# Kernel tuning notes

Measured on AMD Instinct MI355X. Metric: run time of the kernel, lower is better.

Reference implementation:

```python
import jax, jax.numpy as jnp
import numpy as np

N, E, F_IN, F_E = 50000, 800000, 128, 16
R, H, C = 4, 4, 32            # num_relations, heads, out_channels
HC = H * C                     # 128
NEG_SLOPE = 0.2                # PyG RGATConv default negative_slope
EPS = 1e-16                    # PyG softmax epsilon


def rgat_conv(x, src, dst, edge_type, edge_attr, w, q, k, e, le, b, concat):
    """Faithful PyG RGATConv (additive-self-attention, across-relation, dim=1, aggr=add).
    x: [N,F]; w: [R,F,H*C]; q,k,e: [H*C,H]; le: [F_e,H*C]; b: bias."""
    n = x.shape[0]
    xw = jnp.einsum('nf,rfo->rno', x, w)              # [R,N,H*C] per-relation projections
    x_i = xw[edge_type, dst]                          # [E,H*C] target-node proj per edge
    x_j = xw[edge_type, src]                          # [E,H*C] source-node proj per edge
    qi = x_i @ q                                      # [E,H]
    kj = x_j @ k + (edge_attr @ le) @ e               # [E,H] (edge features folded into keys)
    alpha = jax.nn.leaky_relu(qi + kj, NEG_SLOPE)     # [E,H]
    # softmax over incoming edges of each destination node (across relations)
    amax = jax.ops.segment_max(alpha, dst, num_segments=n)
    ex = jnp.exp(alpha - amax[dst])
    denom = jax.ops.segment_sum(ex, dst, num_segments=n)
    alpha = ex / (denom[dst] + EPS)
    msg = alpha[:, :, None] * x_j.reshape(-1, H, C)   # [E,H,C]
    out = jax.ops.segment_sum(msg, dst, num_segments=n)  # [N,H,C] sum aggregation
    out = out.reshape(n, H * C) if concat else out.mean(axis=1)
    return out + b


def setup_inputs() -> dict:
    key = jax.random.key(0)
    ks = jax.random.split(key, 18)
    p = 0.05
    inp = {
        'x': jax.random.normal(ks[0], (N, F_IN), dtype=jnp.float32),
        'edge_index': jax.random.randint(ks[1], (2, E), 0, N, dtype=jnp.int64)
            if jax.config.jax_enable_x64 else jax.random.randint(ks[1], (2, E), 0, N).astype(jnp.int32),
        'edge_attr': jax.random.normal(ks[2], (E, F_E), dtype=jnp.float32),
        'edge_type': jax.random.randint(ks[3], (E,), 0, R).astype(jnp.int32),
        # conv1 params (in=F_IN, concat=True -> bias of size H*C)
        'w1': jax.random.normal(ks[4], (R, F_IN, HC), dtype=jnp.float32) * p,
        'q1': jax.random.normal(ks[5], (HC, H), dtype=jnp.float32) * p,
        'k1': jax.random.normal(ks[6], (HC, H), dtype=jnp.float32) * p,
        'e1': jax.random.normal(ks[7], (HC, H), dtype=jnp.float32) * p,
        'le1': jax.random.normal(ks[8], (F_E, HC), dtype=jnp.float32) * p,
        'b1': jnp.zeros((HC,), dtype=jnp.float32),
        # conv3 params (in=H*C=128, concat=False -> bias of size C)
        'w3': jax.random.normal(ks[9], (R, HC, HC), dtype=jnp.float32) * p,
        'q3': jax.random.normal(ks[10], (HC, H), dtype=jnp.float32) * p,
        'k3': jax.random.normal(ks[11], (HC, H), dtype=jnp.float32) * p,
        'e3': jax.random.normal(ks[12], (HC, H), dtype=jnp.float32) * p,
        'le3': jax.random.normal(ks[13], (F_E, HC), dtype=jnp.float32) * p,
        'b3': jnp.zeros((C,), dtype=jnp.float32),
    }
    return inp


def reference(x, edge_index, edge_attr, edge_type,
              w1, q1, k1, e1, le1, b1,
              w3, q3, k3, e3, le3, b3):
    src, dst = edge_index[0], edge_index[1]
    h = jax.nn.relu(rgat_conv(x, src, dst, edge_type, edge_attr,
                              w1, q1, k1, e1, le1, b1, concat=True))
    out = rgat_conv(h, src, dst, edge_type, edge_attr,
                    w3, q3, k3, e3, le3, b3, concat=False)
    return out
```

## Files before the change

### kernel.cpp

```cpp
#include <hip/hip_runtime.h>


#define NEG_SLOPE 0.2f
#define SOFT_EPS 1e-16f
#define SRC_MASK 0x07FFFFFF

typedef __attribute__((ext_vector_type(8))) short bf16x8;
typedef __attribute__((ext_vector_type(4))) float f32x4;
typedef __attribute__((ext_vector_type(4))) unsigned short u16x4;
typedef __attribute__((ext_vector_type(4))) _Float16 half4;
typedef __attribute__((ext_vector_type(8))) _Float16 half8;

__device__ __forceinline__ void bf16split(float f, unsigned short& h, unsigned short& l) {
  unsigned u = __float_as_uint(f);
  unsigned r = u + 0x7FFFu + ((u >> 16) & 1u);
  h = (unsigned short)(r >> 16);
  float fh = __uint_as_float(((unsigned)h) << 16);
  float d = f - fh;
  unsigned u2 = __float_as_uint(d);
  unsigned r2 = u2 + 0x7FFFu + ((u2 >> 16) & 1u);
  l = (unsigned short)(r2 >> 16);
}


__device__ __forceinline__ void hist_body(int id, const int* __restrict__ dst,
                                          int* __restrict__ deg, int E) {
  int e = id * 256 + (int)threadIdx.x;
  if (e < E) atomicAdd(&deg[dst[e]], 1);
}

__device__ __forceinline__ void convx_body(int id, const float* __restrict__ in,
                                           unsigned short* __restrict__ hi,
                                           unsigned short* __restrict__ lo, int total8) {
  int i = id * 256 + (int)threadIdx.x;
  if (i >= total8) return;
  const float4* p = (const float4*)in + (size_t)i * 2;
  float4 a = p[0], b = p[1];
  float v[8] = {a.x, a.y, a.z, a.w, b.x, b.y, b.z, b.w};
  bf16x8 hv, lv;
#pragma unroll
  for (int j = 0; j < 8; ++j) {
    unsigned short h, l;
    bf16split(v[j], h, l);
    hv[j] = (short)h; lv[j] = (short)l;
  }
  *(bf16x8*)(hi + (size_t)i * 8) = hv;
  *(bf16x8*)(lo + (size_t)i * 8) = lv;
}

__device__ __forceinline__ void ekp_body(int id, const float* __restrict__ ea,
                                         const float* __restrict__ le1, const float* __restrict__ e1,
                                         const float* __restrict__ le3, const float* __restrict__ e3,
                                         float* __restrict__ eks1, float* __restrict__ eks3,
                                         int E) {
  __shared__ float sl[128];
  int t = threadIdx.x;
  if (t < 128) {
    const float* le = (t < 64) ? le1 : le3;
    const float* ee = (t < 64) ? e1 : e3;
    int u = t & 63, f = u >> 2, h = u & 3;
    float acc = 0.f;
    for (int o = 0; o < 128; ++o) acc += le[f * 128 + o] * ee[o * 4 + h];
    sl[t] = acc;
  }
  __syncthreads();
  int i = id * 256 + t;
  if (i >= E) return;
  const float4* a4 = (const float4*)(ea + (size_t)i * 16);
  float a1[4] = {0, 0, 0, 0}, a3[4] = {0, 0, 0, 0};
#pragma unroll
  for (int ii = 0; ii < 4; ++ii) {
    float4 v = a4[ii];
    int f = ii * 4;
#pragma unroll
    for (int h = 0; h < 4; ++h) {
      a1[h] += v.x * sl[f * 4 + h] + v.y * sl[(f + 1) * 4 + h] +
               v.z * sl[(f + 2) * 4 + h] + v.w * sl[(f + 3) * 4 + h];
      a3[h] += v.x * sl[64 + f * 4 + h] + v.y * sl[64 + (f + 1) * 4 + h] +
               v.z * sl[64 + (f + 2) * 4 + h] + v.w * sl[64 + (f + 3) * 4 + h];
    }
  }
  *(float4*)(eks1 + (size_t)i * 4) = make_float4(a1[0], a1[1], a1[2], a1[3]);
  *(float4*)(eks3 + (size_t)i * 4) = make_float4(a3[0], a3[1], a3[2], a3[3]);
}

__device__ __forceinline__ void convw_body(int idx, const float* __restrict__ w1,
                                           const float* __restrict__ w3,
                                           unsigned short* __restrict__ wF1h,
                                           unsigned short* __restrict__ wF1l,
                                           unsigned short* __restrict__ wF3h,
                                           unsigned short* __restrict__ wF3l) {
  if (idx >= 131072) return;
  int L = idx >> 16;
  int rem = idx & 65535;
  int r = rem >> 14, rem2 = rem & 16383, f = rem2 >> 7, o = rem2 & 127;
  const float* w = L ? w3 : w1;
  unsigned short* dh = L ? wF3h : wF1h;
  unsigned short* dl = L ? wF3l : wF1l;
  float v = w[(r * 128 + f) * 128 + o];
  unsigned short h, l;
  bf16split(v, h, l);
  int ot = o >> 4, c = o & 15, kc = f >> 5, q = (f >> 3) & 3, j = f & 7;
  int di = r * 16384 + ((((ot * 4 + kc) * 4 + q) * 16 + c) * 8 + j);
  dh[di] = h;
  dl[di] = l;
}

__device__ __forceinline__ void wqk_body(int idx, const float* __restrict__ w1,
                                         const float* __restrict__ q1, const float* __restrict__ k1,
                                         const float* __restrict__ w3, const float* __restrict__ q3,
                                         const float* __restrict__ k3, float* __restrict__ wqk) {
  if (idx >= 8192) return;
  int L = idx >> 12, rem = idx & 4095;
  int r = rem >> 10, rem2 = rem & 1023, f = rem2 >> 3, j = rem2 & 7;
  const float* w = L ? w3 : w1;
  const float* qk = (j < 4) ? (L ? q3 : q1) : (L ? k3 : k1);
  int h = j & 3;
  const float* wrow = w + (r * 128 + f) * 128;
  float acc = 0.f;
  for (int o = 0; o < 128; ++o) acc += wrow[o] * qk[o * 4 + h];
  wqk[idx] = acc;
}

__global__ __launch_bounds__(256) void pre_kernel(
    const int* __restrict__ dst, int* __restrict__ deg, int E,
    const float* __restrict__ x, unsigned short* __restrict__ xhi,
    unsigned short* __restrict__ xlo, int total8,
    const float* __restrict__ ea,
    const float* __restrict__ le1, const float* __restrict__ e1,
    const float* __restrict__ le3, const float* __restrict__ e3,
    float* __restrict__ eks1, float* __restrict__ eks3,
    const float* __restrict__ w1, const float* __restrict__ q1, const float* __restrict__ k1,
    const float* __restrict__ w3, const float* __restrict__ q3, const float* __restrict__ k3,
    float* __restrict__ wqk,
    unsigned short* __restrict__ wF1h, unsigned short* __restrict__ wF1l,
    unsigned short* __restrict__ wF3h, unsigned short* __restrict__ wF3l,
    int nABC, int eb, int cxb) {
  int bid = blockIdx.x;
  if (bid < nABC) {
    int id = bid / 3, r3 = bid - id * 3;
    if (r3 == 0) {
      if (id < eb) hist_body(id, dst, deg, E);
    } else if (r3 == 1) {
      if (id < cxb) convx_body(id, x, xhi, xlo, total8);
    } else {
      if (id < eb) ekp_body(id, ea, le1, e1, le3, e3, eks1, eks3, E);
    }
  } else {
    int b2 = bid - nABC;
    if (b2 < 512) {
      convw_body(b2 * 256 + (int)threadIdx.x, w1, w3, wF1h, wF1l, wF3h, wF3l);
    } else {
      wqk_body((b2 - 512) * 256 + (int)threadIdx.x, w1, q1, k1, w3, q3, k3, wqk);
    }
  }
}


__global__ __launch_bounds__(256) void scanA_kernel(const int* __restrict__ deg,
                                                    int* __restrict__ bsum, int N) {
  int b = blockIdx.x, t = threadIdx.x;
  int base = b * 1024 + t * 4;
  int s = 0;
#pragma unroll
  for (int j = 0; j < 4; ++j) {
    int i = base + j;
    if (i < N) s += deg[i];
  }
#pragma unroll
  for (int o = 1; o < 64; o <<= 1) s += __shfl_xor(s, o);
  __shared__ int wsum[4];
  if ((t & 63) == 0) wsum[t >> 6] = s;
  __syncthreads();
  if (t == 0) bsum[b] = wsum[0] + wsum[1] + wsum[2] + wsum[3];
}

__global__ __launch_bounds__(256) void scanB_kernel(const int* __restrict__ bsum,
                                                    int* __restrict__ boff,
                                                    int* __restrict__ row_start,
                                                    int nb, int N) {
  int t = threadIdx.x;
  int v = (t < nb) ? bsum[t] : 0;
  int inc = v;
#pragma unroll
  for (int o = 1; o < 64; o <<= 1) {
    int u = __shfl_up(inc, o);
    if ((t & 63) >= o) inc += u;
  }
  __shared__ int wt[4];
  if ((t & 63) == 63) wt[t >> 6] = inc;
  __syncthreads();
  int add = 0;
  for (int wv = 0; wv < (t >> 6); ++wv) add += wt[wv];
  inc += add;
  if (t < nb) boff[t] = inc - v;
  if (t == 255) row_start[N] = inc;
}

__global__ __launch_bounds__(256) void scanC_kernel(const int* __restrict__ deg,
                                                    const int* __restrict__ boff,
                                                    int* __restrict__ row_start,
                                                    int* __restrict__ cursor, int N) {
  int b = blockIdx.x, t = threadIdx.x;
  int base = b * 1024 + t * 4;
  int d[4];
  int s = 0;
#pragma unroll
  for (int j = 0; j < 4; ++j) {
    int i = base + j;
    d[j] = (i < N) ? deg[i] : 0;
    s += d[j];
  }
  int inc = s;
#pragma unroll
  for (int o = 1; o < 64; o <<= 1) {
    int u = __shfl_up(inc, o);
    if ((t & 63) >= o) inc += u;
  }
  __shared__ int wt[4];
  if ((t & 63) == 63) wt[t >> 6] = inc;
  __syncthreads();
  int add = boff[b];
  for (int wv = 0; wv < (t >> 6); ++wv) add += wt[wv];
  int off = add + inc - s;
#pragma unroll
  for (int j = 0; j < 4; ++j) {
    int i = base + j;
    if (i < N) {
      row_start[i] = off;
      cursor[i] = off;
      off += d[j];
    }
  }
}


__device__ __forceinline__ void scatter_body(int id, const int* __restrict__ src,
                                             const int* __restrict__ dst,
                                             const int* __restrict__ et,
                                             int* __restrict__ cursor,
                                             int2* __restrict__ es2, int E) {
  int e = id * 256 + (int)threadIdx.x;
  if (e >= E) return;
  int d = dst[e];
  int pos = atomicAdd(&cursor[d], 1);
  es2[pos] = make_int2(src[e] | (et[e] << 27), e);
}

__device__ __forceinline__ void qkx_body(int nbid, char* smem, const float* __restrict__ xin,
                                         const float* __restrict__ wqk, float* __restrict__ qn,
                                         float* __restrict__ kn, int N) {
  float* swqk = (float*)smem;
  int t = threadIdx.x;
#pragma unroll
  for (int j = 0; j < 16; ++j) {
    int i = j * 256 + t;
    swqk[(i >> 10) * 1032 + (i & 1023)] = wqk[i];
  }
  __syncthreads();
  int nb = nbid * 64;
  int rl = t >> 2, r = t & 3;
  int n = nb + rl;
  int nc = n < N ? n : N - 1;
  const float4* xr = (const float4*)(xin + (size_t)nc * 128);
  const float* wb = swqk + r * 1032;
  float aq0 = 0, aq1 = 0, aq2 = 0, aq3 = 0;
  float ak0 = 0, ak1 = 0, ak2 = 0, ak3 = 0;
#pragma unroll 4
  for (int f4 = 0; f4 < 32; ++f4) {
    float4 xv = xr[f4];
    const float* w0 = wb + f4 * 32;
    float4 qa = *(const float4*)(w0);
    float4 ka = *(const float4*)(w0 + 4);
    float4 qb = *(const float4*)(w0 + 8);
    float4 kb = *(const float4*)(w0 + 12);
    float4 qc = *(const float4*)(w0 + 16);
    float4 kc = *(const float4*)(w0 + 20);
    float4 qd = *(const float4*)(w0 + 24);
    float4 kd = *(const float4*)(w0 + 28);
    aq0 += xv.x * qa.x + xv.y * qb.x + xv.z * qc.x + xv.w * qd.x;
    aq1 += xv.x * qa.y + xv.y * qb.y + xv.z * qc.y + xv.w * qd.y;
    aq2 += xv.x * qa.z + xv.y * qb.z + xv.z * qc.z + xv.w * qd.z;
    aq3 += xv.x * qa.w + xv.y * qb.w + xv.z * qc.w + xv.w * qd.w;
    ak0 += xv.x * ka.x + xv.y * kb.x + xv.z * kc.x + xv.w * kd.x;
    ak1 += xv.x * ka.y + xv.y * kb.y + xv.z * kc.y + xv.w * kd.y;
    ak2 += xv.x * ka.z + xv.y * kb.z + xv.z * kc.z + xv.w * kd.z;
    ak3 += xv.x * ka.w + xv.y * kb.w + xv.z * kc.w + xv.w * kd.w;
  }
  if (n < N) {
    *(float4*)(qn + ((size_t)r * N + n) * 4) = make_float4(aq0, aq1, aq2, aq3);
    *(float4*)(kn + ((size_t)r * N + n) * 4) = make_float4(ak0, ak1, ak2, ak3);
  }
}

__device__ __forceinline__ void proj_body(int pid, char* smem,
                                          const unsigned short* __restrict__ xhi,
                                          const unsigned short* __restrict__ xlo,
                                          const unsigned short* __restrict__ wFh,
                                          const unsigned short* __restrict__ wFl,
                                          _Float16* __restrict__ xwh, int N) {
  bf16x8* wl_h = (bf16x8*)smem;
  bf16x8* wl_l = wl_h + 1024;
  int r = pid & 3;
  int h0 = (pid >> 2) & 1;
  int nb = (pid >> 3) * 128;
  int t = threadIdx.x;
  const bf16x8* srcH = (const bf16x8*)(wFh + r * 16384) + h0 * 1024;
  const bf16x8* srcL = (const bf16x8*)(wFl + r * 16384) + h0 * 1024;
#pragma unroll
  for (int j = 0; j < 4; ++j) {
    int i = j * 256 + t;
    wl_h[i] = srcH[i];
    wl_l[i] = srcL[i];
  }
  __syncthreads();

  int wv = t >> 6;
  int lane = t & 63;
  int c = lane & 15, q = lane >> 4;
  int nodebase = nb + wv * 32;
  int n0 = nodebase + c;
  int n1 = nodebase + 16 + c;
  int n0c = n0 < N ? n0 : N - 1;
  int n1c = n1 < N ? n1 : N - 1;

  f32x4 acc[4][2];
#pragma unroll
  for (int ot = 0; ot < 4; ++ot)
#pragma unroll
    for (int nt = 0; nt < 2; ++nt) acc[ot][nt] = (f32x4){0.f, 0.f, 0.f, 0.f};

  bf16x8 xb[2][4];
  {
    int k0 = q * 8;
    xb[0][0] = *(const bf16x8*)(xhi + (size_t)n0c * 128 + k0);
    xb[0][1] = *(const bf16x8*)(xlo + (size_t)n0c * 128 + k0);
    xb[0][2] = *(const bf16x8*)(xhi + (size_t)n1c * 128 + k0);
    xb[0][3] = *(const bf16x8*)(xlo + (size_t)n1c * 128 + k0);
  }
#pragma unroll
  for (int kc = 0; kc < 4; ++kc) {
    if (kc < 3) {
      int k0 = (kc + 1) * 32 + q * 8;
      xb[(kc + 1) & 1][0] = *(const bf16x8*)(xhi + (size_t)n0c * 128 + k0);
      xb[(kc + 1) & 1][1] = *(const bf16x8*)(xlo + (size_t)n0c * 128 + k0);
      xb[(kc + 1) & 1][2] = *(const bf16x8*)(xhi + (size_t)n1c * 128 + k0);
      xb[(kc + 1) & 1][3] = *(const bf16x8*)(xlo + (size_t)n1c * 128 + k0);
    }
    bf16x8 b0h = xb[kc & 1][0], b0l = xb[kc & 1][1];
    bf16x8 b1h = xb[kc & 1][2], b1l = xb[kc & 1][3];
#pragma unroll
    for (int ot = 0; ot < 4; ++ot) {
      int fi = ((ot * 4 + kc) * 4 + q) * 16 + c;
      bf16x8 ah = wl_h[fi];
      bf16x8 al = wl_l[fi];
      acc[ot][0] = __builtin_amdgcn_mfma_f32_16x16x32_bf16(ah, b0h, acc[ot][0], 0, 0, 0);
      acc[ot][0] = __builtin_amdgcn_mfma_f32_16x16x32_bf16(ah, b0l, acc[ot][0], 0, 0, 0);
      acc[ot][0] = __builtin_amdgcn_mfma_f32_16x16x32_bf16(al, b0h, acc[ot][0], 0, 0, 0);
      acc[ot][1] = __builtin_amdgcn_mfma_f32_16x16x32_bf16(ah, b1h, acc[ot][1], 0, 0, 0);
      acc[ot][1] = __builtin_amdgcn_mfma_f32_16x16x32_bf16(ah, b1l, acc[ot][1], 0, 0, 0);
      acc[ot][1] = __builtin_amdgcn_mfma_f32_16x16x32_bf16(al, b1h, acc[ot][1], 0, 0, 0);
    }
  }

#pragma unroll
  for (int nt = 0; nt < 2; ++nt) {
    int n = nodebase + nt * 16 + c;
    if (n < N) {
      _Float16* basep = xwh + ((size_t)r * N + n) * 128 + h0 * 64 + q * 4;
#pragma unroll
      for (int ot = 0; ot < 4; ++ot) {
        f32x4 a = acc[ot][nt];
        half4 hv;
        hv[0] = (_Float16)a.x; hv[1] = (_Float16)a.y;
        hv[2] = (_Float16)a.z; hv[3] = (_Float16)a.w;
        *(half4*)(basep + ot * 16) = hv;
      }
    }
  }
}

__global__ __launch_bounds__(256) void sc9_kernel(
    const int* __restrict__ src, const int* __restrict__ dst, const int* __restrict__ et,
    int* __restrict__ cursor, int2* __restrict__ es2, int E,
    const float* __restrict__ xin, const float* __restrict__ wqk,
    float* __restrict__ qn, float* __restrict__ kn, int N, int qxb,
    const unsigned short* __restrict__ xhi, const unsigned short* __restrict__ xlo,
    const unsigned short* __restrict__ wFh, const unsigned short* __restrict__ wFl,
    _Float16* __restrict__ xwh, int pjb) {
  extern __shared__ char smem[];
  int bid = blockIdx.x;
  int g = bid / 9, r9 = bid - g * 9;
  if (r9 < 4) {
    scatter_body(g * 4 + r9, src, dst, et, cursor, es2, E);
  } else if (r9 == 4) {
    if (g < qxb) qkx_body(g, smem, xin, wqk, qn, kn, N);
  } else {
    int id = g * 4 + (r9 - 5);
    if (id < pjb) proj_body(id, smem, xhi, xlo, wFh, wFl, xwh, N);
  }
}

__global__ __launch_bounds__(256) void p2_kernel(
    const unsigned short* __restrict__ xhi, const unsigned short* __restrict__ xlo,
    const unsigned short* __restrict__ wFh, const unsigned short* __restrict__ wFl,
    _Float16* __restrict__ xwh, int N,
    const float* __restrict__ xin, const float* __restrict__ wqk,
    float* __restrict__ qn, float* __restrict__ kn, int pjb, int qxb) {
  extern __shared__ char smem[];
  int bid = blockIdx.x;
  int g = bid / 5, r5 = bid - g * 5;
  if (r5 == 4) {
    if (g < qxb) qkx_body(g, smem, xin, wqk, qn, kn, N);
  } else {
    int id = g * 4 + r5;
    if (id < pjb) proj_body(id, smem, xhi, xlo, wFh, wFl, xwh, N);
  }
}


__device__ __forceinline__ float4 edge_alpha(const int2* __restrict__ es2,
                                             const float* __restrict__ qn,
                                             const float* __restrict__ kn,
                                             const float* __restrict__ eks,
                                             int i, int d, int N) {
  int2 v = es2[i];
  int et = (int)((unsigned)v.x >> 27);
  int sn = v.x & SRC_MASK;
  float4 kv = *(const float4*)(kn + (et * N + sn) * 4);
  float4 ev = ((const float4*)eks)[v.y];
  float4 q4 = *(const float4*)(qn + (et * N + d) * 4);
  float4 a = make_float4(q4.x + kv.x + ev.x, q4.y + kv.y + ev.y,
                         q4.z + kv.z + ev.z, q4.w + kv.w + ev.w);
  a.x = a.x > 0.f ? a.x : NEG_SLOPE * a.x;
  a.y = a.y > 0.f ? a.y : NEG_SLOPE * a.y;
  a.z = a.z > 0.f ? a.z : NEG_SLOPE * a.z;
  a.w = a.w > 0.f ? a.w : NEG_SLOPE * a.w;
  return a;
}

__device__ __forceinline__ float4 max4(float4 a, float4 b) {
  return make_float4(fmaxf(a.x, b.x), fmaxf(a.y, b.y), fmaxf(a.z, b.z), fmaxf(a.w, b.w));
}

__global__ __launch_bounds__(256) void agg_kernel(
    const int2* __restrict__ es2, const int* __restrict__ row_start,
    const float* __restrict__ qn, const float* __restrict__ kn,
    const float* __restrict__ eks, float* __restrict__ alpha_s,
    const _Float16* __restrict__ xwh, const float* __restrict__ bias,
    float* __restrict__ out, unsigned short* __restrict__ xhi,
    unsigned short* __restrict__ xlo, int N, int concat) {
  int d = blockIdx.x * 16 + (threadIdx.x >> 4);
  if (d >= N) return;
  int ql = threadIdx.x & 15;
  int rs = row_start[d], re = row_start[d + 1];
  int deg = re - rs;
  int h = ql >> 2;

  float acc[8];
#pragma unroll
  for (int j = 0; j < 8; ++j) acc[j] = 0.f;
  float rden = 0.f;

  if (deg > 0) {
    float4 m = make_float4(-1e30f, -1e30f, -1e30f, -1e30f);
    float4 ar0 = m, ar1 = m, ar2 = m, ar3 = m;
    bool fast = (deg <= 64);
    bool v0 = ql < deg, v1 = 16 + ql < deg, v2 = 32 + ql < deg, v3 = 48 + ql < deg;
    if (fast) {
      int dm1 = deg - 1;
      int o0 = v0 ? ql : dm1;
      int o1 = v1 ? 16 + ql : dm1;
      int o2 = v2 ? 32 + ql : dm1;
      int o3 = v3 ? 48 + ql : dm1;
      float4 a0 = edge_alpha(es2, qn, kn, eks, rs + o0, d, N);
      float4 a1 = edge_alpha(es2, qn, kn, eks, rs + o1, d, N);
      float4 a2 = edge_alpha(es2, qn, kn, eks, rs + o2, d, N);
      float4 a3 = edge_alpha(es2, qn, kn, eks, rs + o3, d, N);
      if (v0) { ar0 = a0; m = max4(m, a0); }
      if (v1) { ar1 = a1; m = max4(m, a1); }
      if (v2) { ar2 = a2; m = max4(m, a2); }
      if (v3) { ar3 = a3; m = max4(m, a3); }
    } else {
      for (int i = rs + ql; i < re; i += 16) {
        float4 a = edge_alpha(es2, qn, kn, eks, i, d, N);
        ((float4*)alpha_s)[i] = a;
        m = max4(m, a);
      }
    }
#pragma unroll
    for (int o = 1; o < 16; o <<= 1) {
      m.x = fmaxf(m.x, __shfl_xor(m.x, o));
      m.y = fmaxf(m.y, __shfl_xor(m.y, o));
      m.z = fmaxf(m.z, __shfl_xor(m.z, o));
      m.w = fmaxf(m.w, __shfl_xor(m.w, o));
    }

    float4 s = make_float4(0.f, 0.f, 0.f, 0.f);
    if (fast) {
#define SWEEPB(V, AR, OFF)                                                   \
      if (V) {                                                               \
        float4 e4 = make_float4(__expf(AR.x - m.x), __expf(AR.y - m.y),      \
                                __expf(AR.z - m.z), __expf(AR.w - m.w));     \
        ((float4*)alpha_s)[rs + OFF + ql] = e4;                              \
        s.x += e4.x; s.y += e4.y; s.z += e4.z; s.w += e4.w;                  \
      }
      SWEEPB(v0, ar0, 0)
      SWEEPB(v1, ar1, 16)
      SWEEPB(v2, ar2, 32)
      SWEEPB(v3, ar3, 48)
#undef SWEEPB
    } else {
      for (int i = rs + ql; i < re; i += 16) {
        float4 a = ((const float4*)alpha_s)[i];
        float4 e4 = make_float4(__expf(a.x - m.x), __expf(a.y - m.y),
                                __expf(a.z - m.z), __expf(a.w - m.w));
        ((float4*)alpha_s)[i] = e4;
        s.x += e4.x; s.y += e4.y; s.z += e4.z; s.w += e4.w;
      }
    }
#pragma unroll
    for (int o = 1; o < 16; o <<= 1) {
      s.x += __shfl_xor(s.x, o); s.y += __shfl_xor(s.y, o);
      s.z += __shfl_xor(s.z, o); s.w += __shfl_xor(s.w, o);
    }
    float smh = (h == 0) ? s.x : (h == 1) ? s.y : (h == 2) ? s.z : s.w;
    rden = 1.f / (smh + SOFT_EPS);

    int e = rs;
    for (; e + 4 <= re; e += 4) {
      int2 a0 = es2[e];
      int2 a1 = es2[e + 1];
      int2 a2 = es2[e + 2];
      int2 a3 = es2[e + 3];
      float w0 = alpha_s[e * 4 + h];
      float w1 = alpha_s[(e + 1) * 4 + h];
      float w2 = alpha_s[(e + 2) * 4 + h];
      float w3 = alpha_s[(e + 3) * 4 + h];
      int p0 = ((int)((unsigned)a0.x >> 27)) * N + (a0.x & SRC_MASK);
      int p1 = ((int)((unsigned)a1.x >> 27)) * N + (a1.x & SRC_MASK);
      int p2 = ((int)((unsigned)a2.x >> 27)) * N + (a2.x & SRC_MASK);
      int p3 = ((int)((unsigned)a3.x >> 27)) * N + (a3.x & SRC_MASK);
      half8 x0 = *(const half8*)(xwh + (size_t)p0 * 128 + ql * 8);
      half8 x1 = *(const half8*)(xwh + (size_t)p1 * 128 + ql * 8);
      half8 x2 = *(const half8*)(xwh + (size_t)p2 * 128 + ql * 8);
      half8 x3 = *(const half8*)(xwh + (size_t)p3 * 128 + ql * 8);
#pragma unroll
      for (int j = 0; j < 8; ++j) {
        acc[j] = fmaf((float)x0[j], w0, acc[j]);
        acc[j] = fmaf((float)x1[j], w1, acc[j]);
        acc[j] = fmaf((float)x2[j], w2, acc[j]);
        acc[j] = fmaf((float)x3[j], w3, acc[j]);
      }
    }
    for (; e < re; ++e) {
      int2 a0 = es2[e];
      float w0 = alpha_s[e * 4 + h];
      int p0 = ((int)((unsigned)a0.x >> 27)) * N + (a0.x & SRC_MASK);
      half8 x0 = *(const half8*)(xwh + (size_t)p0 * 128 + ql * 8);
#pragma unroll
      for (int j = 0; j < 8; ++j) acc[j] = fmaf((float)x0[j], w0, acc[j]);
    }
  }
#pragma unroll
  for (int j = 0; j < 8; ++j) acc[j] *= rden;

  if (concat) {
    float4 b0 = ((const float4*)bias)[ql * 2];
    float4 b1 = ((const float4*)bias)[ql * 2 + 1];
    float v[8] = {acc[0] + b0.x, acc[1] + b0.y, acc[2] + b0.z, acc[3] + b0.w,
                  acc[4] + b1.x, acc[5] + b1.y, acc[6] + b1.z, acc[7] + b1.w};
    u16x4 hv0, lv0, hv1, lv1;
#pragma unroll
    for (int j = 0; j < 8; ++j) {
      v[j] = v[j] > 0.f ? v[j] : 0.f;
      unsigned short hh, ll;
      bf16split(v[j], hh, ll);
      if (j < 4) { hv0[j] = hh; lv0[j] = ll; }
      else { hv1[j - 4] = hh; lv1[j - 4] = ll; }
    }
    float* orow = out + (size_t)d * 128 + ql * 8;
    *(float4*)orow = make_float4(v[0], v[1], v[2], v[3]);
    *(float4*)(orow + 4) = make_float4(v[4], v[5], v[6], v[7]);
    *(u16x4*)(xhi + (size_t)d * 128 + ql * 8) = hv0;
    *(u16x4*)(xhi + (size_t)d * 128 + ql * 8 + 4) = hv1;
    *(u16x4*)(xlo + (size_t)d * 128 + ql * 8) = lv0;
    *(u16x4*)(xlo + (size_t)d * 128 + ql * 8 + 4) = lv1;
  } else {
#pragma unroll
    for (int j = 0; j < 8; ++j) {
      acc[j] += __shfl_xor(acc[j], 4);
      acc[j] += __shfl_xor(acc[j], 8);
    }
    if (ql < 4) {
      float4 b0 = ((const float4*)bias)[ql * 2];
      float4 b1 = ((const float4*)bias)[ql * 2 + 1];
      float* orow = out + (size_t)d * 32 + ql * 8;
      *(float4*)orow = make_float4(0.25f * acc[0] + b0.x, 0.25f * acc[1] + b0.y,
                                   0.25f * acc[2] + b0.z, 0.25f * acc[3] + b0.w);
      *(float4*)(orow + 4) = make_float4(0.25f * acc[4] + b1.x, 0.25f * acc[5] + b1.y,
                                         0.25f * acc[6] + b1.z, 0.25f * acc[7] + b1.w);
    }
  }
}

extern "C" void kernel_launch(void* const* d_in, const int* in_sizes, int n_in,
                              void* d_out, int out_size, void* d_ws, size_t ws_size,
                              hipStream_t stream) {
  const float* x   = (const float*)d_in[0];
  const int*   ei  = (const int*)d_in[1];
  const float* ea  = (const float*)d_in[2];
  const int*   etp = (const int*)d_in[3];
  const float* w1  = (const float*)d_in[4];
  const float* q1  = (const float*)d_in[5];
  const float* k1  = (const float*)d_in[6];
  const float* e1  = (const float*)d_in[7];
  const float* le1 = (const float*)d_in[8];
  const float* b1  = (const float*)d_in[9];
  const float* w3  = (const float*)d_in[10];
  const float* q3  = (const float*)d_in[11];
  const float* k3  = (const float*)d_in[12];
  const float* e3  = (const float*)d_in[13];
  const float* le3 = (const float*)d_in[14];
  const float* b3  = (const float*)d_in[15];
  const int N = in_sizes[0] / 128;
  const int E = in_sizes[3];
  const int* srcp = ei;
  const int* dstp = ei + E;

  float* ws   = (float*)d_ws;
  _Float16* xwh = (_Float16*)ws;
  float* qn   = ws + (size_t)2 * N * 128;
  float* kn   = qn + (size_t)4 * N * 4;
  float* eks1 = kn + (size_t)4 * N * 4;
  float* eks3 = eks1 + (size_t)E * 4;
  float* alph = eks3 + (size_t)E * 4;
  float* hbuf = alph + (size_t)E * 4;
  float* wqkb = hbuf + (size_t)N * 128;
  int* deg      = (int*)(wqkb + 8192);
  int* rowst    = deg + N;
  int* cursor   = rowst + N + 1;
  int* bsum     = cursor + N;
  int* boff     = bsum + 256;
  uintptr_t pe = (uintptr_t)(boff + 256);
  pe = (pe + 15) & ~(uintptr_t)15;
  int2* es2     = (int2*)pe;
  uintptr_t pa = (uintptr_t)(es2 + E);
  pa = (pa + 255) & ~(uintptr_t)255;
  unsigned short* xhi  = (unsigned short*)pa;
  unsigned short* xlo  = xhi + (size_t)N * 128;
  unsigned short* wF1h = xlo + (size_t)N * 128;
  unsigned short* wF1l = wF1h + 4 * 128 * 128;
  unsigned short* wF3h = wF1l + 4 * 128 * 128;
  unsigned short* wF3l = wF3h + 4 * 128 * 128;
  (void)ws_size; (void)n_in; (void)out_size;

  int eb   = (E + 255) / 256;
  int nb16 = (N + 15) / 16;
  int nbs  = (N + 1023) / 1024;
  int pgy  = (N + 127) / 128;
  int pjb  = 8 * pgy;
  int qxb  = (N + 63) / 64;
  int cxb  = (N * 128 / 8 + 255) / 256;

  hipMemsetAsync(deg, 0, (size_t)N * sizeof(int), stream);

  int M = eb > cxb ? eb : cxb;
  int nABC = 3 * M;
  int preg = nABC + 512 + 32;
  pre_kernel<<<preg, 256, 0, stream>>>(dstp, deg, E, x, xhi, xlo, N * 128 / 8,
                                       ea, le1, e1, le3, e3, eks1, eks3,
                                       w1, q1, k1, w3, q3, k3, wqkb,
                                       wF1h, wF1l, wF3h, wF3l, nABC, eb, cxb);
  scanA_kernel<<<nbs, 256, 0, stream>>>(deg, bsum, N);
  scanB_kernel<<<1, 256, 0, stream>>>(bsum, boff, rowst, nbs, N);
  scanC_kernel<<<nbs, 256, 0, stream>>>(deg, boff, rowst, cursor, N);

  int scq = (eb + 3) / 4;
  int pjq = (pjb + 3) / 4;
  int g9 = scq;
  if (qxb > g9) g9 = qxb;
  if (pjq > g9) g9 = pjq;
  sc9_kernel<<<9 * g9, 256, 32768, stream>>>(srcp, dstp, etp, cursor, es2, E,
                                             x, wqkb, qn, kn, N, qxb,
                                             xhi, xlo, wF1h, wF1l, xwh, pjb);

  agg_kernel<<<nb16, 256, 0, stream>>>(es2, rowst, qn, kn, eks1, alph, xwh,
                                       b1, hbuf, xhi, xlo, N, 1);

  int p2grp = pjq > qxb ? pjq : qxb;
  p2_kernel<<<5 * p2grp, 256, 32768, stream>>>(xhi, xlo, wF3h, wF3l, xwh, N,
                                               hbuf, wqkb + 4096, qn, kn, pjb, qxb);

  agg_kernel<<<nb16, 256, 0, stream>>>(es2, rowst, qn, kn, eks3, alph, xwh,
                                       b3, (float*)d_out, xhi, xlo, N, 0);
}
```

Baseline: 436.5 us.

## Pack CSR edge records with pre-permuted edge-key terms for both layers

The scatter step now writes a 64-byte record per sorted edge holding the packed src/type word plus the edge-attribute key contributions for both conv layers, already in destination order. The aggregation kernels read the edge term contiguously from this record instead of gathering it randomly by original edge id. The cost is that the scatter writes 64 bytes per edge instead of 8 and reads eks1/eks3 itself. The aggregation loop also reads a single int at a 64-byte stride, which wastes bandwidth on the gather pass.

```diff
diff --git a/kernel.cpp b/kernel.cpp
--- a/kernel.cpp
+++ b/kernel.cpp
@@ -239,12 +239,20 @@
                                              const int* __restrict__ dst,
                                              const int* __restrict__ et,
                                              int* __restrict__ cursor,
-                                             int2* __restrict__ es2, int E) {
+                                             const float* __restrict__ eks1,
+                                             const float* __restrict__ eks3,
+                                             float* __restrict__ rec, int E) {
   int e = id * 256 + (int)threadIdx.x;
   if (e >= E) return;
+  float4 ev1 = *(const float4*)(eks1 + (size_t)e * 4);
+  float4 ev3 = *(const float4*)(eks3 + (size_t)e * 4);
+  int se = src[e] | (et[e] << 27);
   int d = dst[e];
   int pos = atomicAdd(&cursor[d], 1);
-  es2[pos] = make_int2(src[e] | (et[e] << 27), e);
+  float* rp = rec + (size_t)pos * 16;
+  *(int4*)rp = make_int4(se, 0, 0, 0);
+  *(float4*)(rp + 4) = ev1;
+  *(float4*)(rp + 8) = ev3;
 }
 
 __device__ __forceinline__ void qkx_body(int nbid, char* smem, const float* __restrict__ xin,
@@ -382,7 +390,8 @@
 
 __global__ __launch_bounds__(256) void sc9_kernel(
     const int* __restrict__ src, const int* __restrict__ dst, const int* __restrict__ et,
-    int* __restrict__ cursor, int2* __restrict__ es2, int E,
+    int* __restrict__ cursor, const float* __restrict__ eks1, const float* __restrict__ eks3,
+    float* __restrict__ rec, int E,
     const float* __restrict__ xin, const float* __restrict__ wqk,
     float* __restrict__ qn, float* __restrict__ kn, int N, int qxb,
     const unsigned short* __restrict__ xhi, const unsigned short* __restrict__ xlo,
@@ -392,7 +401,7 @@
   int bid = blockIdx.x;
   int g = bid / 9, r9 = bid - g * 9;
   if (r9 < 4) {
-    scatter_body(g * 4 + r9, src, dst, et, cursor, es2, E);
+    scatter_body(g * 4 + r9, src, dst, et, cursor, eks1, eks3, rec, E);
   } else if (r9 == 4) {
     if (g < qxb) qkx_body(g, smem, xin, wqk, qn, kn, N);
   } else {
@@ -419,16 +428,16 @@
 }
 
 
-__device__ __forceinline__ float4 edge_alpha(const int2* __restrict__ es2,
+__device__ __forceinline__ float4 edge_alpha(const float* __restrict__ rec,
                                              const float* __restrict__ qn,
                                              const float* __restrict__ kn,
-                                             const float* __restrict__ eks,
-                                             int i, int d, int N) {
-  int2 v = es2[i];
-  int et = (int)((unsigned)v.x >> 27);
-  int sn = v.x & SRC_MASK;
+                                             int i, int d, int N, int evo) {
+  const float* rp = rec + (size_t)i * 16;
+  int se = *(const int*)rp;
+  float4 ev = *(const float4*)(rp + evo);
+  int et = (int)((unsigned)se >> 27);
+  int sn = se & SRC_MASK;
   float4 kv = *(const float4*)(kn + (et * N + sn) * 4);
-  float4 ev = ((const float4*)eks)[v.y];
   float4 q4 = *(const float4*)(qn + (et * N + d) * 4);
   float4 a = make_float4(q4.x + kv.x + ev.x, q4.y + kv.y + ev.y,
                          q4.z + kv.z + ev.z, q4.w + kv.w + ev.w);
@@ -444,12 +453,12 @@
 }
 
 __global__ __launch_bounds__(256) void agg_kernel(
-    const int2* __restrict__ es2, const int* __restrict__ row_start,
+    const float* __restrict__ rec, const int* __restrict__ row_start,
     const float* __restrict__ qn, const float* __restrict__ kn,
-    const float* __restrict__ eks, float* __restrict__ alpha_s,
+    float* __restrict__ alpha_s,
     const _Float16* __restrict__ xwh, const float* __restrict__ bias,
     float* __restrict__ out, unsigned short* __restrict__ xhi,
-    unsigned short* __restrict__ xlo, int N, int concat) {
+    unsigned short* __restrict__ xlo, int N, int concat, int evo) {
   int d = blockIdx.x * 16 + (threadIdx.x >> 4);
   if (d >= N) return;
   int ql = threadIdx.x & 15;
@@ -473,17 +482,17 @@
       int o1 = v1 ? 16 + ql : dm1;
       int o2 = v2 ? 32 + ql : dm1;
       int o3 = v3 ? 48 + ql : dm1;
-      float4 a0 = edge_alpha(es2, qn, kn, eks, rs + o0, d, N);
-      float4 a1 = edge_alpha(es2, qn, kn, eks, rs + o1, d, N);
-      float4 a2 = edge_alpha(es2, qn, kn, eks, rs + o2, d, N);
-      float4 a3 = edge_alpha(es2, qn, kn, eks, rs + o3, d, N);
+      float4 a0 = edge_alpha(rec, qn, kn, rs + o0, d, N, evo);
+      float4 a1 = edge_alpha(rec, qn, kn, rs + o1, d, N, evo);
+      float4 a2 = edge_alpha(rec, qn, kn, rs + o2, d, N, evo);
+      float4 a3 = edge_alpha(rec, qn, kn, rs + o3, d, N, evo);
       if (v0) { ar0 = a0; m = max4(m, a0); }
       if (v1) { ar1 = a1; m = max4(m, a1); }
       if (v2) { ar2 = a2; m = max4(m, a2); }
       if (v3) { ar3 = a3; m = max4(m, a3); }
     } else {
       for (int i = rs + ql; i < re; i += 16) {
-        float4 a = edge_alpha(es2, qn, kn, eks, i, d, N);
+        float4 a = edge_alpha(rec, qn, kn, i, d, N, evo);
         ((float4*)alpha_s)[i] = a;
         m = max4(m, a);
       }
@@ -529,18 +538,18 @@
 
     int e = rs;
     for (; e + 4 <= re; e += 4) {
-      int2 a0 = es2[e];
-      int2 a1 = es2[e + 1];
-      int2 a2 = es2[e + 2];
-      int2 a3 = es2[e + 3];
+      int se0 = *(const int*)(rec + (size_t)e * 16);
+      int se1 = *(const int*)(rec + (size_t)(e + 1) * 16);
+      int se2 = *(const int*)(rec + (size_t)(e + 2) * 16);
+      int se3 = *(const int*)(rec + (size_t)(e + 3) * 16);
       float w0 = alpha_s[e * 4 + h];
       float w1 = alpha_s[(e + 1) * 4 + h];
       float w2 = alpha_s[(e + 2) * 4 + h];
       float w3 = alpha_s[(e + 3) * 4 + h];
-      int p0 = ((int)((unsigned)a0.x >> 27)) * N + (a0.x & SRC_MASK);
-      int p1 = ((int)((unsigned)a1.x >> 27)) * N + (a1.x & SRC_MASK);
-      int p2 = ((int)((unsigned)a2.x >> 27)) * N + (a2.x & SRC_MASK);
-      int p3 = ((int)((unsigned)a3.x >> 27)) * N + (a3.x & SRC_MASK);
+      int p0 = ((int)((unsigned)se0 >> 27)) * N + (se0 & SRC_MASK);
+      int p1 = ((int)((unsigned)se1 >> 27)) * N + (se1 & SRC_MASK);
+      int p2 = ((int)((unsigned)se2 >> 27)) * N + (se2 & SRC_MASK);
+      int p3 = ((int)((unsigned)se3 >> 27)) * N + (se3 & SRC_MASK);
       half8 x0 = *(const half8*)(xwh + (size_t)p0 * 128 + ql * 8);
       half8 x1 = *(const half8*)(xwh + (size_t)p1 * 128 + ql * 8);
       half8 x2 = *(const half8*)(xwh + (size_t)p2 * 128 + ql * 8);
@@ -554,9 +563,9 @@
       }
     }
     for (; e < re; ++e) {
-      int2 a0 = es2[e];
+      int se0 = *(const int*)(rec + (size_t)e * 16);
       float w0 = alpha_s[e * 4 + h];
-      int p0 = ((int)((unsigned)a0.x >> 27)) * N + (a0.x & SRC_MASK);
+      int p0 = ((int)((unsigned)se0 >> 27)) * N + (se0 & SRC_MASK);
       half8 x0 = *(const half8*)(xwh + (size_t)p0 * 128 + ql * 8);
 #pragma unroll
       for (int j = 0; j < 8; ++j) acc[j] = fmaf((float)x0[j], w0, acc[j]);
@@ -643,9 +652,9 @@
   int* bsum     = cursor + N;
   int* boff     = bsum + 256;
   uintptr_t pe = (uintptr_t)(boff + 256);
-  pe = (pe + 15) & ~(uintptr_t)15;
-  int2* es2     = (int2*)pe;
-  uintptr_t pa = (uintptr_t)(es2 + E);
+  pe = (pe + 63) & ~(uintptr_t)63;
+  float* rec    = (float*)pe;
+  uintptr_t pa = (uintptr_t)(rec + (size_t)E * 16);
   pa = (pa + 255) & ~(uintptr_t)255;
   unsigned short* xhi  = (unsigned short*)pa;
   unsigned short* xlo  = xhi + (size_t)N * 128;
@@ -681,17 +690,17 @@
   int g9 = scq;
   if (qxb > g9) g9 = qxb;
   if (pjq > g9) g9 = pjq;
-  sc9_kernel<<<9 * g9, 256, 32768, stream>>>(srcp, dstp, etp, cursor, es2, E,
-                                             x, wqkb, qn, kn, N, qxb,
+  sc9_kernel<<<9 * g9, 256, 32768, stream>>>(srcp, dstp, etp, cursor, eks1, eks3,
+                                             rec, E, x, wqkb, qn, kn, N, qxb,
                                              xhi, xlo, wF1h, wF1l, xwh, pjb);
 
-  agg_kernel<<<nb16, 256, 0, stream>>>(es2, rowst, qn, kn, eks1, alph, xwh,
-                                       b1, hbuf, xhi, xlo, N, 1);
+  agg_kernel<<<nb16, 256, 0, stream>>>(rec, rowst, qn, kn, alph, xwh,
+                                       b1, hbuf, xhi, xlo, N, 1, 4);
 
   int p2grp = pjq > qxb ? pjq : qxb;
   p2_kernel<<<5 * p2grp, 256, 32768, stream>>>(xhi, xlo, wF3h, wF3l, xwh, N,
                                                hbuf, wqkb + 4096, qn, kn, pjb, qxb);
 
-  agg_kernel<<<nb16, 256, 0, stream>>>(es2, rowst, qn, kn, eks3, alph, xwh,
-                                       b3, (float*)d_out, xhi, xlo, N, 0);
-}
+  agg_kernel<<<nb16, 256, 0, stream>>>(rec, rowst, qn, kn, alph, xwh,
+                                       b3, (float*)d_out, xhi, xlo, N, 0, 8);
+}
```

Measured after the change: 441.8 us. Within noise of the previous version (+1.2%).
